# Kernel optimization log

Hardware: AMD Instinct MI355X
Metric: run time of the kernel (lower is better)

The kernel has to match this reference:

```python
import jax, jax.numpy as jnp
import numpy as np

N_NODES = 50000
N_EDGES = 800000
IN_CH = 128
OUT_CH = 64  # hidden = 2*OUT_CH = 128


def setup_inputs() -> dict:
    key = jax.random.key(0)
    ks = jax.random.split(key, 5)
    x = jax.random.normal(ks[0], (N_NODES, IN_CH), dtype=jnp.float32)
    edge_index = jax.random.randint(ks[1], (2, N_EDGES), 0, N_NODES, dtype=jnp.int32)
    # Glorot-ish scaled weights for the two GCNConv layers
    W1 = jax.random.normal(ks[2], (IN_CH, 2 * OUT_CH), dtype=jnp.float32) * 0.05
    b1 = jnp.zeros((2 * OUT_CH,), dtype=jnp.float32)
    W2 = jax.random.normal(ks[3], (2 * OUT_CH, OUT_CH), dtype=jnp.float32) * 0.05
    b2 = jnp.zeros((OUT_CH,), dtype=jnp.float32)
    return {"x": x, "edge_index": edge_index, "W1": W1, "b1": b1, "W2": W2, "b2": b2}


def reference(x, edge_index, W1, b1, W2, b2):
    N = x.shape[0]
    # GCN normalization with self-loops (PyG GCNConv default):
    # A_hat = A + I, deg from target nodes, norm = d_i^-1/2 * d_j^-1/2
    loops = jnp.arange(N, dtype=edge_index.dtype)
    row = jnp.concatenate([edge_index[0], loops])  # source
    col = jnp.concatenate([edge_index[1], loops])  # target
    deg = jax.ops.segment_sum(jnp.ones(row.shape, x.dtype), col, num_segments=N)
    dinv = jnp.where(deg > 0, jax.lax.rsqrt(deg), 0.0)
    norm = dinv[row] * dinv[col]  # [E+N]

    def conv(h, W, b):
        h = h @ W                           # [N, D_out] transform first (D_out <= D_in path)
        msg = norm[:, None] * h[row]        # gather + scale: [E+N, D_out]
        agg = jax.ops.segment_sum(msg, col, num_segments=N)
        return agg + b

    h = jax.nn.relu(conv(x, W1, b1))
    return conv(h, W2, b2)
```

## Files before the change

kernel.cpp:

```cpp
#include <hip/hip_runtime.h>
#include <hip/hip_bf16.h>
#include <hip/hip_fp16.h>

#define IN_CH  128
#define HID    128
#define OUTC   64

#define NSCAT 256
#define SLOTC 64
#define CAPB  7168
#define CAP2  7168
#define TSTRIDE 140

typedef _Float16 half8 __attribute__((ext_vector_type(8)));
typedef _Float16 half4v __attribute__((ext_vector_type(4)));
typedef float float4v __attribute__((ext_vector_type(4)));

__device__ __forceinline__ void vacc(float4v& a0, float4v& a1, half8 u) {
    half4v lo = __builtin_shufflevector(u, u, 0, 1, 2, 3);
    half4v hi = __builtin_shufflevector(u, u, 4, 5, 6, 7);
    a0 += __builtin_convertvector(lo, float4v);
    a1 += __builtin_convertvector(hi, float4v);
}
__device__ __forceinline__ void vaccw(float4v& a0, float4v& a1, half8 u, float w) {
    half4v lo = __builtin_shufflevector(u, u, 0, 1, 2, 3);
    half4v hi = __builtin_shufflevector(u, u, 4, 5, 6, 7);
    a0 += w * __builtin_convertvector(lo, float4v);
    a1 += w * __builtin_convertvector(hi, float4v);
}

__global__ __launch_bounds__(256) void scatA_kernel(
        const int* __restrict__ src, const int* __restrict__ dst,
        unsigned* __restrict__ tmp2, ushort* __restrict__ cnts,
        const float* __restrict__ W1, const float* __restrict__ W2,
        _Float16* __restrict__ Wt1, _Float16* __restrict__ Wt2,
        int E, int N, int NBK) {
    __shared__ int cnt[256];
    int t = threadIdx.x, blk = blockIdx.x;
    cnt[t] = 0;
    __syncthreads();
    int E4 = E >> 2;
    for (int q = blk * 256 + t; q < E4; q += NSCAT * 256) {
        int4 s4 = ((const int4*)src)[q];
        int4 d4 = ((const int4*)dst)[q];
        {
            int b = ((unsigned)d4.x) >> 8;
            int pos = atomicAdd(&cnt[b], 1);
            if (pos < SLOTC)
                tmp2[((size_t)(b << 8) + blk) * SLOTC + pos] = (((unsigned)d4.x) << 16) | (unsigned)s4.x;
        }
        {
            int b = ((unsigned)d4.y) >> 8;
            int pos = atomicAdd(&cnt[b], 1);
            if (pos < SLOTC)
                tmp2[((size_t)(b << 8) + blk) * SLOTC + pos] = (((unsigned)d4.y) << 16) | (unsigned)s4.y;
        }
        {
            int b = ((unsigned)d4.z) >> 8;
            int pos = atomicAdd(&cnt[b], 1);
            if (pos < SLOTC)
                tmp2[((size_t)(b << 8) + blk) * SLOTC + pos] = (((unsigned)d4.z) << 16) | (unsigned)s4.z;
        }
        {
            int b = ((unsigned)d4.w) >> 8;
            int pos = atomicAdd(&cnt[b], 1);
            if (pos < SLOTC)
                tmp2[((size_t)(b << 8) + blk) * SLOTC + pos] = (((unsigned)d4.w) << 16) | (unsigned)s4.w;
        }
    }
    if (blk == 0 && t < (E & 3)) {
        int e = (E4 << 2) + t;
        unsigned d = (unsigned)dst[e], s = (unsigned)src[e];
        int b = d >> 8;
        int pos = atomicAdd(&cnt[b], 1);
        if (pos < SLOTC)
            tmp2[((size_t)(b << 8) + blk) * SLOTC + pos] = (d << 16) | s;
    }
    __syncthreads();
    if (t < NBK) {
        int c = cnt[t]; if (c > SLOTC) c = SLOTC;
        cnts[t * 256 + blk] = (ushort)c;
    }

    for (int idx = blk * 256 + t; idx < 128 * 128 + 128 * 64; idx += NSCAT * 256) {
        if (idx < 128 * 128) {
            int k = idx >> 7, nn = idx & 127;
            Wt1[nn * 128 + k] = (_Float16)W1[idx];
        } else {
            int j = idx - 128 * 128;
            int k = j >> 6, nn = j & 63;
            Wt2[nn * 128 + k] = (_Float16)W2[j];
        }
    }
}

__global__ __launch_bounds__(256) void csrB_kernel(
        const unsigned* __restrict__ tmp2, const ushort* __restrict__ cnts,
        int* __restrict__ off, ushort* __restrict__ degs, float* __restrict__ dinv,
        ushort* __restrict__ srcs,
        const float* __restrict__ x, _Float16* __restrict__ xh,
        int N, int NBK) {
    __shared__ int ex[257];
    __shared__ int hcnt[256], cur[256];
    __shared__ unsigned ein[CAP2];
    __shared__ ushort outb[CAP2];
    __shared__ float dsh[256];
    __shared__ int wsum[4], wsum2[4], atot_s;
    int b = blockIdx.x, t = threadIdx.x;
    int lane = t & 63, wid = t >> 6;

    int c = cnts[b * 256 + t];
    int x1 = c;
#pragma unroll
    for (int d = 1; d < 64; d <<= 1) {
        int y = __shfl_up(x1, d, 64);
        if (lane >= d) x1 += y;
    }
    if (lane == 63) wsum[wid] = x1;
    __syncthreads();
    {
        int add = 0;
        for (int k = 0; k < wid; ++k) add += wsum[k];
        x1 += add;
    }
    ex[t] = x1 - c;
    if (t == 255) ex[256] = x1;
    __syncthreads();
    int total = ex[256]; if (total > CAP2) total = CAP2;

    for (int i = t; i < total; i += 256) {
        int lo = 0, hi = 255;
        while (lo < hi) {
            int mid = (lo + hi + 1) >> 1;
            if (ex[mid] <= i) lo = mid; else hi = mid - 1;
        }
        ein[i] = tmp2[((size_t)(b << 8) + lo) * SLOTC + (i - ex[lo])];
    }
    __syncthreads();

    hcnt[t] = 0;
    __syncthreads();
    for (int i = t; i < total; i += 256)
        atomicAdd(&hcnt[(ein[i] >> 16) & 255], 1);
    __syncthreads();
    int cdeg = hcnt[t];
    int adeg = (cdeg + 7) & ~7;

    int x2 = adeg;
#pragma unroll
    for (int d = 1; d < 64; d <<= 1) {
        int y = __shfl_up(x2, d, 64);
        if (lane >= d) x2 += y;
    }
    if (lane == 63) wsum2[wid] = x2;
    __syncthreads();
    {
        int add = 0;
        for (int k = 0; k < wid; ++k) add += wsum2[k];
        x2 += add;
    }
    int excl = x2 - adeg;
    if (t == 255) atot_s = x2;

    int node = (b << 8) + t;
    float dv = rsqrtf((float)(cdeg + 1));
    if (node < N) {
        off[node] = b * CAPB + excl;
        degs[node] = (ushort)cdeg;
        dinv[node] = dv;
    }
    dsh[t] = (node < N) ? dv : 0.f;
    cur[t] = excl;
    __syncthreads();
    for (int i = t; i < total; i += 256) {
        unsigned v = ein[i];
        int pos = atomicAdd(&cur[(v >> 16) & 255], 1);
        outb[pos] = (ushort)(v & 0xFFFFu);
    }
    __syncthreads();
    for (int k = excl + cdeg; k < excl + adeg; ++k) outb[k] = (ushort)node;
    __syncthreads();
    int atot = atot_s;
    for (int i = t; i < atot; i += 256) srcs[b * CAPB + i] = outb[i];

    int rowbase = b << 8;
    for (int m = t; m < 256 * 16; m += 256) {
        int r = m >> 4, k = m & 15;
        int nd = rowbase + r;
        if (nd < N) {
            const float4* xp = (const float4*)(x + (size_t)nd * 128 + k * 8);
            float4 v0 = xp[0], v1 = xp[1];
            float di = dsh[r];
            half8 o = { (_Float16)(di * v0.x), (_Float16)(di * v0.y),
                        (_Float16)(di * v0.z), (_Float16)(di * v0.w),
                        (_Float16)(di * v1.x), (_Float16)(di * v1.y),
                        (_Float16)(di * v1.z), (_Float16)(di * v1.w) };
            ((half8*)xh)[(size_t)nd * 16 + k] = o;
        }
    }
}

__global__ __launch_bounds__(256, 8) void agg1_kernel(const _Float16* __restrict__ xh,
                                                      const int* __restrict__ off,
                                                      const ushort* __restrict__ degs,
                                                      const ushort* __restrict__ srcs,
                                                      const float* __restrict__ dinv,
                                                      _Float16* __restrict__ A1, int N) {
    int grp = threadIdx.x >> 4;
    int p   = threadIdx.x & 15;
    int node = blockIdx.x * 16 + grp;
    if (node >= N) return;
    int s = off[node];
    int deg = degs[node];
    int adeg = (deg + 7) & ~7;
    int pcnt = adeg - deg;

    const half8* xs = (const half8*)xh;
    float4v a0 = (float4v)0.f, a1 = (float4v)0.f;
    float4v c0 = (float4v)0.f, c1 = (float4v)0.f;

    const uint4* sp = (const uint4*)(srcs + s);
    int nr = adeg >> 3;
    for (int r = 0; r < nr; ++r) {
        uint4 iv = sp[r];
        int i0 = iv.x & 0xFFFF, i1 = iv.x >> 16;
        int i2 = iv.y & 0xFFFF, i3 = iv.y >> 16;
        int i4 = iv.z & 0xFFFF, i5 = iv.z >> 16;
        int i6 = iv.w & 0xFFFF, i7 = iv.w >> 16;
        half8 u0 = xs[(size_t)i0 * 16 + p];
        half8 u1 = xs[(size_t)i1 * 16 + p];
        half8 u2 = xs[(size_t)i2 * 16 + p];
        half8 u3 = xs[(size_t)i3 * 16 + p];
        half8 u4 = xs[(size_t)i4 * 16 + p];
        half8 u5 = xs[(size_t)i5 * 16 + p];
        half8 u6 = xs[(size_t)i6 * 16 + p];
        half8 u7 = xs[(size_t)i7 * 16 + p];
        vacc(a0, a1, u0); vacc(c0, c1, u1);
        vacc(a0, a1, u2); vacc(c0, c1, u3);
        vacc(a0, a1, u4); vacc(c0, c1, u5);
        vacc(a0, a1, u6); vacc(c0, c1, u7);
    }
    a0 += c0; a1 += c1;

    float di = dinv[node];
    half8 sv = xs[(size_t)node * 16 + p];
    vaccw(a0, a1, sv, (float)(1 - pcnt));
    a0 *= di; a1 *= di;
    half4v h0 = __builtin_convertvector(a0, half4v);
    half4v h1 = __builtin_convertvector(a1, half4v);
    half8 hh = __builtin_shufflevector(h0, h1, 0, 1, 2, 3, 4, 5, 6, 7);
    *((half8*)(A1 + (size_t)node * 128) + p) = hh;
}

__global__ __launch_bounds__(256) void gemm_fused_kernel(
        const _Float16* __restrict__ A1, const _Float16* __restrict__ Wt1,
        const float* __restrict__ b1, const _Float16* __restrict__ Wt2,
        const float* __restrict__ dinv, _Float16* __restrict__ H3s, int N) {
    __shared__ _Float16 tile[4][32 * TSTRIDE];
    int wave = threadIdx.x >> 6;
    int lane = threadIdx.x & 63;
    int n16 = lane & 15;
    int q   = lane >> 4;
    int rowBase = blockIdx.x * 128 + wave * 32;

    half8 a[2][4];
#pragma unroll
    for (int rt = 0; rt < 2; ++rt) {
        int row = rowBase + rt * 16 + n16;
        if (row >= N) row = N - 1;
        const _Float16* ap = A1 + (size_t)row * 128 + q * 8;
#pragma unroll
        for (int kb = 0; kb < 4; ++kb)
            a[rt][kb] = *(const half8*)(ap + kb * 32);
    }

    float4v acc1[2][8];
#pragma unroll
    for (int rt = 0; rt < 2; ++rt)
#pragma unroll
        for (int ct = 0; ct < 8; ++ct) acc1[rt][ct] = (float4v)0.f;
#pragma unroll
    for (int ct = 0; ct < 8; ++ct) {
        const _Float16* bp = Wt1 + (size_t)(ct * 16 + n16) * 128 + q * 8;
        half8 b[4];
#pragma unroll
        for (int kb = 0; kb < 4; ++kb) b[kb] = *(const half8*)(bp + kb * 32);
#pragma unroll
        for (int kb = 0; kb < 4; ++kb) {
            acc1[0][ct] = __builtin_amdgcn_mfma_f32_16x16x32_f16(a[0][kb], b[kb], acc1[0][ct], 0, 0, 0);
            acc1[1][ct] = __builtin_amdgcn_mfma_f32_16x16x32_f16(a[1][kb], b[kb], acc1[1][ct], 0, 0, 0);
        }
    }

    _Float16* tw = &tile[wave][0];
#pragma unroll
    for (int ct = 0; ct < 8; ++ct) {
        int col = ct * 16 + n16;
        float bv = b1[col];
#pragma unroll
        for (int rt = 0; rt < 2; ++rt)
#pragma unroll
            for (int r = 0; r < 4; ++r) {
                int row = rt * 16 + q * 4 + r;
                tw[row * TSTRIDE + col] = (_Float16)fmaxf(acc1[rt][ct][r] + bv, 0.f);
            }
    }
    __syncthreads();

    half8 a2[2][4];
#pragma unroll
    for (int rt = 0; rt < 2; ++rt) {
        const _Float16* tp = tw + (rt * 16 + n16) * TSTRIDE + q * 8;
#pragma unroll
        for (int kb = 0; kb < 4; ++kb)
            a2[rt][kb] = *(const half8*)(tp + kb * 32);
    }

    float4v acc2[2][4];
#pragma unroll
    for (int rt = 0; rt < 2; ++rt)
#pragma unroll
        for (int ct = 0; ct < 4; ++ct) acc2[rt][ct] = (float4v)0.f;
#pragma unroll
    for (int ct = 0; ct < 4; ++ct) {
        const _Float16* bp = Wt2 + (size_t)(ct * 16 + n16) * 128 + q * 8;
        half8 b[4];
#pragma unroll
        for (int kb = 0; kb < 4; ++kb) b[kb] = *(const half8*)(bp + kb * 32);
#pragma unroll
        for (int kb = 0; kb < 4; ++kb) {
            acc2[0][ct] = __builtin_amdgcn_mfma_f32_16x16x32_f16(a2[0][kb], b[kb], acc2[0][ct], 0, 0, 0);
            acc2[1][ct] = __builtin_amdgcn_mfma_f32_16x16x32_f16(a2[1][kb], b[kb], acc2[1][ct], 0, 0, 0);
        }
    }

#pragma unroll
    for (int rt = 0; rt < 2; ++rt)
#pragma unroll
        for (int ct = 0; ct < 4; ++ct) {
            int col = ct * 16 + n16;
#pragma unroll
            for (int r = 0; r < 4; ++r) {
                int row = rowBase + rt * 16 + q * 4 + r;
                if (row < N)
                    H3s[(size_t)row * OUTC + col] = (_Float16)(acc2[rt][ct][r] * dinv[row]);
            }
        }
}

__global__ __launch_bounds__(256, 8) void agg2_kernel(const _Float16* __restrict__ H3s,
                                                      const int* __restrict__ off,
                                                      const ushort* __restrict__ degs,
                                                      const ushort* __restrict__ srcs,
                                                      const float* __restrict__ dinv,
                                                      const float* __restrict__ bias,
                                                      float* __restrict__ out, int N) {
    int grp = threadIdx.x >> 3;
    int p   = threadIdx.x & 7;
    int node = blockIdx.x * 32 + grp;
    if (node >= N) return;
    int s = off[node];
    int deg = degs[node];
    int adeg = (deg + 7) & ~7;
    int pcnt = adeg - deg;

    const half8* hs = (const half8*)H3s;
    float4v a0 = (float4v)0.f, a1 = (float4v)0.f;
    float4v c0 = (float4v)0.f, c1 = (float4v)0.f;

    const uint4* sp = (const uint4*)(srcs + s);
    int nr = adeg >> 3;
    for (int r = 0; r < nr; ++r) {
        uint4 iv = sp[r];
        int i0 = iv.x & 0xFFFF, i1 = iv.x >> 16;
        int i2 = iv.y & 0xFFFF, i3 = iv.y >> 16;
        int i4 = iv.z & 0xFFFF, i5 = iv.z >> 16;
        int i6 = iv.w & 0xFFFF, i7 = iv.w >> 16;
        half8 u0 = hs[(size_t)i0 * 8 + p];
        half8 u1 = hs[(size_t)i1 * 8 + p];
        half8 u2 = hs[(size_t)i2 * 8 + p];
        half8 u3 = hs[(size_t)i3 * 8 + p];
        half8 u4 = hs[(size_t)i4 * 8 + p];
        half8 u5 = hs[(size_t)i5 * 8 + p];
        half8 u6 = hs[(size_t)i6 * 8 + p];
        half8 u7 = hs[(size_t)i7 * 8 + p];
        vacc(a0, a1, u0); vacc(c0, c1, u1);
        vacc(a0, a1, u2); vacc(c0, c1, u3);
        vacc(a0, a1, u4); vacc(c0, c1, u5);
        vacc(a0, a1, u6); vacc(c0, c1, u7);
    }
    a0 += c0; a1 += c1;

    float di = dinv[node];
    half8 sv = hs[(size_t)node * 8 + p];
    vaccw(a0, a1, sv, (float)(1 - pcnt));
    const float4v* bp = (const float4v*)(bias + p * 8);
    float4v o0 = di * a0 + bp[0];
    float4v o1 = di * a1 + bp[1];
    float4v* op = (float4v*)(out + (size_t)node * 64 + p * 8);
    op[0] = o0; op[1] = o1;
}

extern "C" void kernel_launch(void* const* d_in, const int* in_sizes, int n_in,
                              void* d_out, int out_size, void* d_ws, size_t ws_size,
                              hipStream_t stream) {
    const float* x   = (const float*)d_in[0];
    const int*   ei  = (const int*)d_in[1];
    const float* W1  = (const float*)d_in[2];
    const float* b1  = (const float*)d_in[3];
    const float* W2  = (const float*)d_in[4];
    const float* b2  = (const float*)d_in[5];
    float* out = (float*)d_out;

    const int N = in_sizes[0] / IN_CH;
    const int E = in_sizes[1] / 2;
    const int* src = ei;
    const int* dst = ei + E;

    const int NBK = (N + 255) >> 8;

    auto align256 = [](size_t v) { return (v + 255) & ~(size_t)255; };
    char* w = (char*)d_ws;
    int* off = (int*)w;              w += align256((size_t)N * 4);
    ushort* degs = (ushort*)w;       w += align256((size_t)N * 2);
    float* dinv = (float*)w;         w += align256((size_t)N * 4);
    ushort* cnts = (ushort*)w;       w += align256((size_t)NBK * 256 * 2);
    ushort* srcs = (ushort*)w;       w += align256((size_t)NBK * CAPB * 2);
    _Float16* Wt1 = (_Float16*)w;    w += align256((size_t)HID * 128 * 2);
    _Float16* Wt2 = (_Float16*)w;    w += align256((size_t)OUTC * 128 * 2);
    size_t reg1 = align256((size_t)NBK * 256 * SLOTC * 4);
    if (reg1 < align256((size_t)N * HID * 2)) reg1 = align256((size_t)N * HID * 2);
    unsigned* tmp2 = (unsigned*)w;
    _Float16* A1 = (_Float16*)w;     w += reg1;
    _Float16* xh = (_Float16*)w;
    _Float16* H3s = (_Float16*)w;    w += align256((size_t)N * HID * 2);

    scatA_kernel<<<NSCAT, 256, 0, stream>>>(src, dst, tmp2, cnts,
                                            W1, W2, Wt1, Wt2, E, N, NBK);
    csrB_kernel<<<NBK, 256, 0, stream>>>(tmp2, cnts, off, degs, dinv, srcs,
                                         x, xh, N, NBK);

    agg1_kernel<<<(N + 15) / 16, 256, 0, stream>>>(xh, off, degs, srcs, dinv, A1, N);
    gemm_fused_kernel<<<(N + 127) / 128, 256, 0, stream>>>(A1, Wt1, b1, Wt2, dinv, H3s, N);
    agg2_kernel<<<(N + 31) / 32, 256, 0, stream>>>(H3s, off, degs, srcs, dinv, b2, out, N);
}
```

Measured before the change: 178.1 us.

## Sort nodes by degree bucket within each block to balance aggregation warps

The CSR build kernel now counting-sorts the 256 nodes of each block by padded degree bucket and writes a permutation array. Both aggregation kernels map their thread groups through this permutation, so nodes with similar degree share a wavefront and divergence in loop trip count is reduced. Grid sizes change to cover whole 256-node blocks, and nodes at or beyond N are skipped by the existing bound check. This adds a shared histogram, one extra permutation read per node, and less contiguous output writes.

```diff
diff --git a/kernel.cpp b/kernel.cpp
--- a/kernel.cpp
+++ b/kernel.cpp
@@ -97,7 +97,7 @@
 __global__ __launch_bounds__(256) void csrB_kernel(
         const unsigned* __restrict__ tmp2, const ushort* __restrict__ cnts,
         int* __restrict__ off, ushort* __restrict__ degs, float* __restrict__ dinv,
-        ushort* __restrict__ srcs,
+        ushort* __restrict__ srcs, ushort* __restrict__ perm,
         const float* __restrict__ x, _Float16* __restrict__ xh,
         int N, int NBK) {
     __shared__ int ex[257];
@@ -106,6 +106,7 @@
     __shared__ ushort outb[CAP2];
     __shared__ float dsh[256];
     __shared__ int wsum[4], wsum2[4], atot_s;
+    __shared__ int dhist[17], dcur[16];
     int b = blockIdx.x, t = threadIdx.x;
     int lane = t & 63, wid = t >> 6;
 
@@ -117,6 +118,7 @@
         if (lane >= d) x1 += y;
     }
     if (lane == 63) wsum[wid] = x1;
+    if (t < 17) dhist[t] = 0;
     __syncthreads();
     {
         int add = 0;
@@ -146,6 +148,9 @@
     int cdeg = hcnt[t];
     int adeg = (cdeg + 7) & ~7;
 
+    int bin = adeg >> 3; if (bin > 15) bin = 15;
+    atomicAdd(&dhist[bin + 1], 1);
+
     int x2 = adeg;
 #pragma unroll
     for (int d = 1; d < 64; d <<= 1) {
@@ -161,6 +166,13 @@
     }
     int excl = x2 - adeg;
     if (t == 255) atot_s = x2;
+    if (t == 0) {
+        int acc = 0;
+#pragma unroll
+        for (int k = 0; k < 16; ++k) { acc += dhist[k + 1]; dhist[k + 1] = acc; }
+#pragma unroll
+        for (int k = 0; k < 16; ++k) dcur[k] = dhist[k];
+    }
 
     int node = (b << 8) + t;
     float dv = rsqrtf((float)(cdeg + 1));
@@ -172,6 +184,12 @@
     dsh[t] = (node < N) ? dv : 0.f;
     cur[t] = excl;
     __syncthreads();
+
+    {
+        int rank = atomicAdd(&dcur[bin], 1);
+        perm[(b << 8) + rank] = (ushort)t;
+    }
+
     for (int i = t; i < total; i += 256) {
         unsigned v = ein[i];
         int pos = atomicAdd(&cur[(v >> 16) & 255], 1);
@@ -205,10 +223,12 @@
                                                       const ushort* __restrict__ degs,
                                                       const ushort* __restrict__ srcs,
                                                       const float* __restrict__ dinv,
+                                                      const ushort* __restrict__ perm,
                                                       _Float16* __restrict__ A1, int N) {
     int grp = threadIdx.x >> 4;
     int p   = threadIdx.x & 15;
-    int node = blockIdx.x * 16 + grp;
+    int vi = blockIdx.x * 16 + grp;
+    int node = ((vi >> 8) << 8) + perm[vi];
     if (node >= N) return;
     int s = off[node];
     int deg = degs[node];
@@ -353,11 +373,13 @@
                                                       const ushort* __restrict__ degs,
                                                       const ushort* __restrict__ srcs,
                                                       const float* __restrict__ dinv,
+                                                      const ushort* __restrict__ perm,
                                                       const float* __restrict__ bias,
                                                       float* __restrict__ out, int N) {
     int grp = threadIdx.x >> 3;
     int p   = threadIdx.x & 7;
-    int node = blockIdx.x * 32 + grp;
+    int vi = blockIdx.x * 32 + grp;
+    int node = ((vi >> 8) << 8) + perm[vi];
     if (node >= N) return;
     int s = off[node];
     int deg = degs[node];
@@ -426,6 +448,7 @@
     float* dinv = (float*)w;         w += align256((size_t)N * 4);
     ushort* cnts = (ushort*)w;       w += align256((size_t)NBK * 256 * 2);
     ushort* srcs = (ushort*)w;       w += align256((size_t)NBK * CAPB * 2);
+    ushort* perm = (ushort*)w;       w += align256((size_t)NBK * 256 * 2);
     _Float16* Wt1 = (_Float16*)w;    w += align256((size_t)HID * 128 * 2);
     _Float16* Wt2 = (_Float16*)w;    w += align256((size_t)OUTC * 128 * 2);
     size_t reg1 = align256((size_t)NBK * 256 * SLOTC * 4);
@@ -437,10 +460,10 @@
 
     scatA_kernel<<<NSCAT, 256, 0, stream>>>(src, dst, tmp2, cnts,
                                             W1, W2, Wt1, Wt2, E, N, NBK);
-    csrB_kernel<<<NBK, 256, 0, stream>>>(tmp2, cnts, off, degs, dinv, srcs,
+    csrB_kernel<<<NBK, 256, 0, stream>>>(tmp2, cnts, off, degs, dinv, srcs, perm,
                                          x, xh, N, NBK);
 
-    agg1_kernel<<<(N + 15) / 16, 256, 0, stream>>>(xh, off, degs, srcs, dinv, A1, N);
+    agg1_kernel<<<NBK * 16, 256, 0, stream>>>(xh, off, degs, srcs, dinv, perm, A1, N);
     gemm_fused_kernel<<<(N + 127) / 128, 256, 0, stream>>>(A1, Wt1, b1, Wt2, dinv, H3s, N);
-    agg2_kernel<<<(N + 31) / 32, 256, 0, stream>>>(H3s, off, degs, srcs, dinv, b2, out, N);
-}
+    agg2_kernel<<<NBK * 8, 256, 0, stream>>>(H3s, off, degs, srcs, dinv, perm, b2, out, N);
+}
```

Measured after the change: 181.5 us. About the same (+1.9%).

## Merge edge scatter and CSR build into one cooperative kernel with grid sync

Applied to the files above, without the earlier changes.

Fuses the edge-bucketing scatter kernel and the CSR-building kernel into a single cooperative launch with NBK blocks, separated by a grid-wide barrier. It removes one kernel launch and the gap between the two kernels. In exchange the scatter phase now runs on NBK (196) blocks instead of 256, and cnts entries for unused slots are zeroed explicitly. The cooperative launch needs every block resident at once, which the large shared-memory footprint per block could constrain.

```diff
diff --git a/kernel.cpp b/kernel.cpp
--- a/kernel.cpp
+++ b/kernel.cpp
@@ -1,12 +1,14 @@
 #include <hip/hip_runtime.h>
+#include <hip/hip_cooperative_groups.h>
 #include <hip/hip_bf16.h>
 #include <hip/hip_fp16.h>
+
+namespace cg = cooperative_groups;
 
 #define IN_CH  128
 #define HID    128
 #define OUTC   64
 
-#define NSCAT 256
 #define SLOTC 64
 #define CAPB  7168
 #define CAP2  7168
@@ -29,77 +31,15 @@
     a1 += w * __builtin_convertvector(hi, float4v);
 }
 
-__global__ __launch_bounds__(256) void scatA_kernel(
+__global__ __launch_bounds__(256) void build_kernel(
         const int* __restrict__ src, const int* __restrict__ dst,
         unsigned* __restrict__ tmp2, ushort* __restrict__ cnts,
+        int* __restrict__ off, ushort* __restrict__ degs, float* __restrict__ dinv,
+        ushort* __restrict__ srcs,
+        const float* __restrict__ x, _Float16* __restrict__ xh,
         const float* __restrict__ W1, const float* __restrict__ W2,
         _Float16* __restrict__ Wt1, _Float16* __restrict__ Wt2,
         int E, int N, int NBK) {
-    __shared__ int cnt[256];
-    int t = threadIdx.x, blk = blockIdx.x;
-    cnt[t] = 0;
-    __syncthreads();
-    int E4 = E >> 2;
-    for (int q = blk * 256 + t; q < E4; q += NSCAT * 256) {
-        int4 s4 = ((const int4*)src)[q];
-        int4 d4 = ((const int4*)dst)[q];
-        {
-            int b = ((unsigned)d4.x) >> 8;
-            int pos = atomicAdd(&cnt[b], 1);
-            if (pos < SLOTC)
-                tmp2[((size_t)(b << 8) + blk) * SLOTC + pos] = (((unsigned)d4.x) << 16) | (unsigned)s4.x;
-        }
-        {
-            int b = ((unsigned)d4.y) >> 8;
-            int pos = atomicAdd(&cnt[b], 1);
-            if (pos < SLOTC)
-                tmp2[((size_t)(b << 8) + blk) * SLOTC + pos] = (((unsigned)d4.y) << 16) | (unsigned)s4.y;
-        }
-        {
-            int b = ((unsigned)d4.z) >> 8;
-            int pos = atomicAdd(&cnt[b], 1);
-            if (pos < SLOTC)
-                tmp2[((size_t)(b << 8) + blk) * SLOTC + pos] = (((unsigned)d4.z) << 16) | (unsigned)s4.z;
-        }
-        {
-            int b = ((unsigned)d4.w) >> 8;
-            int pos = atomicAdd(&cnt[b], 1);
-            if (pos < SLOTC)
-                tmp2[((size_t)(b << 8) + blk) * SLOTC + pos] = (((unsigned)d4.w) << 16) | (unsigned)s4.w;
-        }
-    }
-    if (blk == 0 && t < (E & 3)) {
-        int e = (E4 << 2) + t;
-        unsigned d = (unsigned)dst[e], s = (unsigned)src[e];
-        int b = d >> 8;
-        int pos = atomicAdd(&cnt[b], 1);
-        if (pos < SLOTC)
-            tmp2[((size_t)(b << 8) + blk) * SLOTC + pos] = (d << 16) | s;
-    }
-    __syncthreads();
-    if (t < NBK) {
-        int c = cnt[t]; if (c > SLOTC) c = SLOTC;
-        cnts[t * 256 + blk] = (ushort)c;
-    }
-
-    for (int idx = blk * 256 + t; idx < 128 * 128 + 128 * 64; idx += NSCAT * 256) {
-        if (idx < 128 * 128) {
-            int k = idx >> 7, nn = idx & 127;
-            Wt1[nn * 128 + k] = (_Float16)W1[idx];
-        } else {
-            int j = idx - 128 * 128;
-            int k = j >> 6, nn = j & 63;
-            Wt2[nn * 128 + k] = (_Float16)W2[j];
-        }
-    }
-}
-
-__global__ __launch_bounds__(256) void csrB_kernel(
-        const unsigned* __restrict__ tmp2, const ushort* __restrict__ cnts,
-        int* __restrict__ off, ushort* __restrict__ degs, float* __restrict__ dinv,
-        ushort* __restrict__ srcs,
-        const float* __restrict__ x, _Float16* __restrict__ xh,
-        int N, int NBK) {
     __shared__ int ex[257];
     __shared__ int hcnt[256], cur[256];
     __shared__ unsigned ein[CAP2];
@@ -108,6 +48,64 @@
     __shared__ int wsum[4], wsum2[4], atot_s;
     int b = blockIdx.x, t = threadIdx.x;
     int lane = t & 63, wid = t >> 6;
+
+    hcnt[t] = 0;
+    if (t >= NBK) cnts[b * 256 + t] = 0;
+    __syncthreads();
+    int E4 = E >> 2;
+    for (int q = b * 256 + t; q < E4; q += NBK * 256) {
+        int4 s4 = ((const int4*)src)[q];
+        int4 d4 = ((const int4*)dst)[q];
+        {
+            int bk = ((unsigned)d4.x) >> 8;
+            int pos = atomicAdd(&hcnt[bk], 1);
+            if (pos < SLOTC)
+                tmp2[((size_t)(bk << 8) + b) * SLOTC + pos] = (((unsigned)d4.x) << 16) | (unsigned)s4.x;
+        }
+        {
+            int bk = ((unsigned)d4.y) >> 8;
+            int pos = atomicAdd(&hcnt[bk], 1);
+            if (pos < SLOTC)
+                tmp2[((size_t)(bk << 8) + b) * SLOTC + pos] = (((unsigned)d4.y) << 16) | (unsigned)s4.y;
+        }
+        {
+            int bk = ((unsigned)d4.z) >> 8;
+            int pos = atomicAdd(&hcnt[bk], 1);
+            if (pos < SLOTC)
+                tmp2[((size_t)(bk << 8) + b) * SLOTC + pos] = (((unsigned)d4.z) << 16) | (unsigned)s4.z;
+        }
+        {
+            int bk = ((unsigned)d4.w) >> 8;
+            int pos = atomicAdd(&hcnt[bk], 1);
+            if (pos < SLOTC)
+                tmp2[((size_t)(bk << 8) + b) * SLOTC + pos] = (((unsigned)d4.w) << 16) | (unsigned)s4.w;
+        }
+    }
+    if (b == 0 && t < (E & 3)) {
+        int e = (E4 << 2) + t;
+        unsigned d = (unsigned)dst[e], s = (unsigned)src[e];
+        int bk = d >> 8;
+        int pos = atomicAdd(&hcnt[bk], 1);
+        if (pos < SLOTC)
+            tmp2[((size_t)(bk << 8) + b) * SLOTC + pos] = (d << 16) | s;
+    }
+    __syncthreads();
+    if (t < NBK) {
+        int c = hcnt[t]; if (c > SLOTC) c = SLOTC;
+        cnts[t * 256 + b] = (ushort)c;
+    }
+    for (int idx = b * 256 + t; idx < 128 * 128 + 128 * 64; idx += NBK * 256) {
+        if (idx < 128 * 128) {
+            int k = idx >> 7, nn = idx & 127;
+            Wt1[nn * 128 + k] = (_Float16)W1[idx];
+        } else {
+            int j = idx - 128 * 128;
+            int k = j >> 6, nn = j & 63;
+            Wt2[nn * 128 + k] = (_Float16)W2[j];
+        }
+    }
+
+    cg::this_grid().sync();
 
     int c = cnts[b * 256 + t];
     int x1 = c;
@@ -435,10 +433,14 @@
     _Float16* xh = (_Float16*)w;
     _Float16* H3s = (_Float16*)w;    w += align256((size_t)N * HID * 2);
 
-    scatA_kernel<<<NSCAT, 256, 0, stream>>>(src, dst, tmp2, cnts,
-                                            W1, W2, Wt1, Wt2, E, N, NBK);
-    csrB_kernel<<<NBK, 256, 0, stream>>>(tmp2, cnts, off, degs, dinv, srcs,
-                                         x, xh, N, NBK);
+    int Ev = E, Nv = N, NBKv = NBK;
+    void* kargs[] = { (void*)&src, (void*)&dst, (void*)&tmp2, (void*)&cnts,
+                      (void*)&off, (void*)&degs, (void*)&dinv, (void*)&srcs,
+                      (void*)&x, (void*)&xh, (void*)&W1, (void*)&W2,
+                      (void*)&Wt1, (void*)&Wt2,
+                      (void*)&Ev, (void*)&Nv, (void*)&NBKv };
+    hipLaunchCooperativeKernel((void*)build_kernel, dim3(NBK), dim3(256),
+                               kargs, 0, stream);
 
     agg1_kernel<<<(N + 15) / 16, 256, 0, stream>>>(xh, off, degs, srcs, dinv, A1, N);
     gemm_fused_kernel<<<(N + 127) / 128, 256, 0, stream>>>(A1, Wt1, b1, Wt2, dinv, H3s, N);
```

Result: slower. 223.0 us (+25.2%).

## Split feature tables into column slabs so each gather pass stays cache-resident

Applied to the files above, without the earlier changes.

Stores the fp16 scaled input features and the layer-2 hidden features in a column-slab layout: 4 slabs of 32 channels for layer 1 and 2 slabs for layer 2, each slab contiguous over nodes. The aggregation kernels now map each block to one slab and 64 nodes, with 4 threads per node, and interleave block IDs so concurrent blocks share a slab. The aim is a smaller random-gather working set per pass that fits in L2/MALL, cutting DRAM traffic for the irregular neighbor reads. In exchange, the CSR index list is read once per slab instead of once overall, and each gathered row is narrower (64 bytes).

```diff
diff --git a/kernel.cpp b/kernel.cpp
--- a/kernel.cpp
+++ b/kernel.cpp
@@ -186,6 +186,7 @@
     int rowbase = b << 8;
     for (int m = t; m < 256 * 16; m += 256) {
         int r = m >> 4, k = m & 15;
+        int q = k >> 2, kk = k & 3;
         int nd = rowbase + r;
         if (nd < N) {
             const float4* xp = (const float4*)(x + (size_t)nd * 128 + k * 8);
@@ -195,7 +196,7 @@
                         (_Float16)(di * v0.z), (_Float16)(di * v0.w),
                         (_Float16)(di * v1.x), (_Float16)(di * v1.y),
                         (_Float16)(di * v1.z), (_Float16)(di * v1.w) };
-            ((half8*)xh)[(size_t)nd * 16 + k] = o;
+            ((half8*)xh)[((size_t)q * N + nd) * 4 + kk] = o;
         }
     }
 }
@@ -206,16 +207,19 @@
                                                       const ushort* __restrict__ srcs,
                                                       const float* __restrict__ dinv,
                                                       _Float16* __restrict__ A1, int N) {
-    int grp = threadIdx.x >> 4;
-    int p   = threadIdx.x & 15;
-    int node = blockIdx.x * 16 + grp;
+    int bid = blockIdx.x;
+    int q = (bid >> 1) & 3;
+    int nb = (bid >> 3) * 2 + (bid & 1);
+    int grp = threadIdx.x >> 2;
+    int p   = threadIdx.x & 3;
+    int node = nb * 64 + grp;
     if (node >= N) return;
     int s = off[node];
     int deg = degs[node];
     int adeg = (deg + 7) & ~7;
     int pcnt = adeg - deg;
 
-    const half8* xs = (const half8*)xh;
+    const half8* xs = (const half8*)xh + (size_t)q * N * 4;
     float4v a0 = (float4v)0.f, a1 = (float4v)0.f;
     float4v c0 = (float4v)0.f, c1 = (float4v)0.f;
 
@@ -227,14 +231,14 @@
         int i2 = iv.y & 0xFFFF, i3 = iv.y >> 16;
         int i4 = iv.z & 0xFFFF, i5 = iv.z >> 16;
         int i6 = iv.w & 0xFFFF, i7 = iv.w >> 16;
-        half8 u0 = xs[(size_t)i0 * 16 + p];
-        half8 u1 = xs[(size_t)i1 * 16 + p];
-        half8 u2 = xs[(size_t)i2 * 16 + p];
-        half8 u3 = xs[(size_t)i3 * 16 + p];
-        half8 u4 = xs[(size_t)i4 * 16 + p];
-        half8 u5 = xs[(size_t)i5 * 16 + p];
-        half8 u6 = xs[(size_t)i6 * 16 + p];
-        half8 u7 = xs[(size_t)i7 * 16 + p];
+        half8 u0 = xs[(size_t)i0 * 4 + p];
+        half8 u1 = xs[(size_t)i1 * 4 + p];
+        half8 u2 = xs[(size_t)i2 * 4 + p];
+        half8 u3 = xs[(size_t)i3 * 4 + p];
+        half8 u4 = xs[(size_t)i4 * 4 + p];
+        half8 u5 = xs[(size_t)i5 * 4 + p];
+        half8 u6 = xs[(size_t)i6 * 4 + p];
+        half8 u7 = xs[(size_t)i7 * 4 + p];
         vacc(a0, a1, u0); vacc(c0, c1, u1);
         vacc(a0, a1, u2); vacc(c0, c1, u3);
         vacc(a0, a1, u4); vacc(c0, c1, u5);
@@ -243,13 +247,13 @@
     a0 += c0; a1 += c1;
 
     float di = dinv[node];
-    half8 sv = xs[(size_t)node * 16 + p];
+    half8 sv = xs[(size_t)node * 4 + p];
     vaccw(a0, a1, sv, (float)(1 - pcnt));
     a0 *= di; a1 *= di;
     half4v h0 = __builtin_convertvector(a0, half4v);
     half4v h1 = __builtin_convertvector(a1, half4v);
     half8 hh = __builtin_shufflevector(h0, h1, 0, 1, 2, 3, 4, 5, 6, 7);
-    *((half8*)(A1 + (size_t)node * 128) + p) = hh;
+    *(half8*)(A1 + (size_t)node * 128 + q * 32 + p * 8) = hh;
 }
 
 __global__ __launch_bounds__(256) void gemm_fused_kernel(
@@ -339,11 +343,12 @@
 #pragma unroll
         for (int ct = 0; ct < 4; ++ct) {
             int col = ct * 16 + n16;
+            int hh2 = col >> 5, cw = col & 31;
 #pragma unroll
             for (int r = 0; r < 4; ++r) {
                 int row = rowBase + rt * 16 + q * 4 + r;
                 if (row < N)
-                    H3s[(size_t)row * OUTC + col] = (_Float16)(acc2[rt][ct][r] * dinv[row]);
+                    H3s[((size_t)hh2 * N + row) * 32 + cw] = (_Float16)(acc2[rt][ct][r] * dinv[row]);
             }
         }
 }
@@ -355,16 +360,19 @@
                                                       const float* __restrict__ dinv,
                                                       const float* __restrict__ bias,
                                                       float* __restrict__ out, int N) {
-    int grp = threadIdx.x >> 3;
-    int p   = threadIdx.x & 7;
-    int node = blockIdx.x * 32 + grp;
+    int bid = blockIdx.x;
+    int h = (bid >> 2) & 1;
+    int nb = (bid >> 3) * 4 + (bid & 3);
+    int grp = threadIdx.x >> 2;
+    int p   = threadIdx.x & 3;
+    int node = nb * 64 + grp;
     if (node >= N) return;
     int s = off[node];
     int deg = degs[node];
     int adeg = (deg + 7) & ~7;
     int pcnt = adeg - deg;
 
-    const half8* hs = (const half8*)H3s;
+    const half8* hs = (const half8*)H3s + (size_t)h * N * 4;
     float4v a0 = (float4v)0.f, a1 = (float4v)0.f;
     float4v c0 = (float4v)0.f, c1 = (float4v)0.f;
 
@@ -376,14 +384,14 @@
         int i2 = iv.y & 0xFFFF, i3 = iv.y >> 16;
         int i4 = iv.z & 0xFFFF, i5 = iv.z >> 16;
         int i6 = iv.w & 0xFFFF, i7 = iv.w >> 16;
-        half8 u0 = hs[(size_t)i0 * 8 + p];
-        half8 u1 = hs[(size_t)i1 * 8 + p];
-        half8 u2 = hs[(size_t)i2 * 8 + p];
-        half8 u3 = hs[(size_t)i3 * 8 + p];
-        half8 u4 = hs[(size_t)i4 * 8 + p];
-        half8 u5 = hs[(size_t)i5 * 8 + p];
-        half8 u6 = hs[(size_t)i6 * 8 + p];
-        half8 u7 = hs[(size_t)i7 * 8 + p];
+        half8 u0 = hs[(size_t)i0 * 4 + p];
+        half8 u1 = hs[(size_t)i1 * 4 + p];
+        half8 u2 = hs[(size_t)i2 * 4 + p];
+        half8 u3 = hs[(size_t)i3 * 4 + p];
+        half8 u4 = hs[(size_t)i4 * 4 + p];
+        half8 u5 = hs[(size_t)i5 * 4 + p];
+        half8 u6 = hs[(size_t)i6 * 4 + p];
+        half8 u7 = hs[(size_t)i7 * 4 + p];
         vacc(a0, a1, u0); vacc(c0, c1, u1);
         vacc(a0, a1, u2); vacc(c0, c1, u3);
         vacc(a0, a1, u4); vacc(c0, c1, u5);
@@ -392,12 +400,13 @@
     a0 += c0; a1 += c1;
 
     float di = dinv[node];
-    half8 sv = hs[(size_t)node * 8 + p];
+    half8 sv = hs[(size_t)node * 4 + p];
     vaccw(a0, a1, sv, (float)(1 - pcnt));
-    const float4v* bp = (const float4v*)(bias + p * 8);
-    float4v o0 = di * a0 + bp[0];
-    float4v o1 = di * a1 + bp[1];
-    float4v* op = (float4v*)(out + (size_t)node * 64 + p * 8);
+    const float* bp = bias + h * 32 + p * 8;
+    float4v b0 = ((const float4v*)bp)[0], b1 = ((const float4v*)bp)[1];
+    float4v o0 = di * a0 + b0;
+    float4v o1 = di * a1 + b1;
+    float4v* op = (float4v*)(out + (size_t)node * 64 + h * 32 + p * 8);
     op[0] = o0; op[1] = o1;
 }
 
@@ -440,7 +449,10 @@
     csrB_kernel<<<NBK, 256, 0, stream>>>(tmp2, cnts, off, degs, dinv, srcs,
                                          x, xh, N, NBK);
 
-    agg1_kernel<<<(N + 15) / 16, 256, 0, stream>>>(xh, off, degs, srcs, dinv, A1, N);
+    const int NB64 = (N + 63) / 64;
+    const int grid1 = ((NB64 + 1) / 2) * 8;
+    const int grid2 = ((NB64 + 3) / 4) * 8;
+    agg1_kernel<<<grid1, 256, 0, stream>>>(xh, off, degs, srcs, dinv, A1, N);
     gemm_fused_kernel<<<(N + 127) / 128, 256, 0, stream>>>(A1, Wt1, b1, Wt2, dinv, H3s, N);
-    agg2_kernel<<<(N + 31) / 32, 256, 0, stream>>>(H3s, off, degs, srcs, dinv, b2, out, N);
-}
+    agg2_kernel<<<grid2, 256, 0, stream>>>(H3s, off, degs, srcs, dinv, b2, out, N);
+}
```

Result: no change. 178.4 us (+0.2%).
